# Kernel optimization log

Measured on AMD Instinct MI355X. Metric: run time of the kernel, lower is better.

Reference implementation:

```python
import jax, jax.numpy as jnp
import numpy as np

N_NODES = 8192
N_EDGES = 262144
FEAT = 128


def _lin(key, fan_in, fan_out):
    k1, k2 = jax.random.split(key)
    s = 1.0 / np.sqrt(fan_in)
    w = jax.random.uniform(k1, (fan_in, fan_out), jnp.float32, -s, s)
    b = jax.random.uniform(k2, (fan_out,), jnp.float32, -s, s)
    return w, b


def setup_inputs() -> dict:
    key = jax.random.key(0)
    ks = jax.random.split(key, 16)
    adj = jax.random.randint(ks[0], (2, N_EDGES), 0, N_NODES)
    features = jax.random.normal(ks[1], (N_NODES, FEAT), jnp.float32)
    w1, b1 = _lin(ks[2], FEAT, 64)
    w2, b2 = _lin(ks[3], 64, 32)
    w3, b3 = _lin(ks[4], 32, 32)
    # MultiheadAttention params (embed_dim=32, 1 head)
    kq = jax.random.split(ks[5], 2)
    wqkv = jax.random.uniform(kq[0], (96, 32), jnp.float32, -1/np.sqrt(32), 1/np.sqrt(32))
    bqkv = jnp.zeros((96,), jnp.float32)
    wo = jax.random.uniform(kq[1], (32, 32), jnp.float32, -1/np.sqrt(32), 1/np.sqrt(32))
    bo = jnp.zeros((32,), jnp.float32)
    w4, b4 = _lin(ks[6], 32, 32)
    w5a, b5a = _lin(ks[7], 32, 32)
    w6a, b6a = _lin(ks[8], 32, 64)
    w7a, b7a = _lin(ks[9], 64, 2)
    w5f, b5f = _lin(ks[10], 32, 32)
    w6f, b6f = _lin(ks[11], 32, 64)
    w7f, b7f = _lin(ks[12], 64, FEAT)
    return dict(adj=adj, features=features, w1=w1, b1=b1, w2=w2, b2=b2, w3=w3, b3=b3,
                wqkv=wqkv, bqkv=bqkv, wo=wo, bo=bo, w4=w4, b4=b4,
                w5a=w5a, b5a=b5a, w6a=w6a, b6a=b6a, w7a=w7a, b7a=b7a,
                w5f=w5f, b5f=b5f, w6f=w6f, b6f=b6f, w7f=w7f, b7f=b7f)


def _gcn(x, w, b, src, dst, norm, n):
    # PyG GCNConv: out = scatter_add(norm * (x W)[src] -> dst) + b
    h = x @ w
    return jax.ops.segment_sum(h[src] * norm[:, None], dst, num_segments=n) + b


def reference(adj, features, w1, b1, w2, b2, w3, b3, wqkv, bqkv, wo, bo, w4, b4,
              w5a, b5a, w6a, b6a, w7a, b7a, w5f, b5f, w6f, b6f, w7f, b7f):
    n = features.shape[0]
    loops = jnp.arange(n)
    src = jnp.concatenate([adj[0], loops])  # self-loops added (gcn_norm)
    dst = jnp.concatenate([adj[1], loops])
    deg = jax.ops.segment_sum(jnp.ones_like(src, jnp.float32), dst, num_segments=n)
    dinv = jnp.where(deg > 0, jax.lax.rsqrt(deg), 0.0)
    norm = dinv[src] * dinv[dst]

    h = jax.nn.relu(_gcn(features, w1, b1, src, dst, norm, n))
    h = jax.nn.relu(_gcn(h, w2, b2, src, dst, norm, n))
    h = jax.nn.relu(_gcn(h, w3, b3, src, dst, norm, n))

    # single-head self-attention over all nodes (seq_len=n, batch=1)
    qkv = h @ wqkv.T + bqkv
    q, k, v = jnp.split(qkv, 3, axis=-1)  # [n,32] each
    attn = jax.nn.softmax((q @ k.T) * (1.0 / np.sqrt(32.0)), axis=-1)  # [n,n]
    h = (attn @ v) @ wo.T + bo

    h = jax.nn.relu(_gcn(h, w4, b4, src, dst, norm, n))

    da = jax.nn.relu(_gcn(h, w5a, b5a, src, dst, norm, n))
    da = jax.nn.relu(_gcn(da, w6a, b6a, src, dst, norm, n))
    da = jax.nn.relu(_gcn(da, w7a, b7a, src, dst, norm, n))  # [n,2]

    df = jax.nn.relu(_gcn(h, w5f, b5f, src, dst, norm, n))
    df = jax.nn.relu(_gcn(df, w6f, b6f, src, dst, norm, n))
    df = jax.nn.relu(_gcn(df, w7f, b7f, src, dst, norm, n))  # [n,FEAT]
    return (da, df)
```

## Files before the change

### kernel.cpp

```cpp
#include <hip/hip_runtime.h>

#define N_NODES 8192
#define N_EDGES 262144

typedef __attribute__((ext_vector_type(4))) float f32x4;
typedef _Float16 half8 __attribute__((ext_vector_type(8)));
typedef _Float16 half4v __attribute__((ext_vector_type(4)));
typedef __fp16 fp16x2 __attribute__((ext_vector_type(2)));
union UH { half8 h8; fp16x2 h2[4]; };
union HC { _Float16 h; unsigned short u; };


__global__ void __launch_bounds__(256) zero_kernel(int4* __restrict__ p) {
  p[blockIdx.x * 256 + threadIdx.x] = make_int4(0, 0, 0, 0);
}


__global__ void __launch_bounds__(256) count_kernel(const int* __restrict__ dst,
                                                    int* __restrict__ cnt) {
  int e = blockIdx.x * 256 + threadIdx.x;
  atomicAdd(&cnt[dst[e]], 1);
}

__global__ void __launch_bounds__(1024) scan_kernel(const int* __restrict__ cnt,
                                                    int* __restrict__ rp,
                                                    float* __restrict__ dinv) {
  __shared__ int sums[1024];
  const int t = threadIdx.x;
  const int base = t * 8;
  int c[8];
  int s = 0;
#pragma unroll
  for (int i = 0; i < 8; ++i) { c[i] = cnt[base + i]; s += c[i]; }
  sums[t] = s;
  __syncthreads();
  for (int off = 1; off < 1024; off <<= 1) {
    int v = (t >= off) ? sums[t - off] : 0;
    __syncthreads();
    sums[t] += v;
    __syncthreads();
  }
  int run = (t == 0) ? 0 : sums[t - 1];
#pragma unroll
  for (int i = 0; i < 8; ++i) {
    rp[base + i] = run;
    run += c[i];
    dinv[base + i] = rsqrtf((float)(c[i] + 1));
  }
  if (t == 1023) rp[N_NODES] = run;
}

__global__ void __launch_bounds__(256) fill_kernel(const int* __restrict__ src,
                                                   const int* __restrict__ dst,
                                                   const int* __restrict__ rp,
                                                   const float* __restrict__ dinv,
                                                   int* __restrict__ cur,
                                                   int* __restrict__ col,
                                                   float* __restrict__ wgt) {
  int e = blockIdx.x * 256 + threadIdx.x;
  int d = dst[e], s = src[e];
  int p = atomicAdd(&cur[d], 1);
  int at = rp[d] + p;
  col[at] = s;
  wgt[at] = dinv[s] * dinv[d];
}


template <int FIN, int FOUT, bool WT, bool BIAS, bool RELU, bool O16>
__device__ __forceinline__ void mm_body(const float* __restrict__ x,
                                        const float* __restrict__ w,
                                        const float* __restrict__ bias, void* out,
                                        int bx, int tid, float* ws, float* xs) {
  constexpr int VEC = (FOUT >= 32) ? 4 : 1;
  constexpr int TC = FOUT / VEC;
  constexpr int ROWS = 256 / TC;
  const int r0 = bx * ROWS;
  for (int i = tid; i < FIN * FOUT; i += 256) {
    int k = i / FOUT, j = i % FOUT;
    ws[i] = WT ? w[j * FIN + k] : w[i];
  }
  for (int i = tid; i < ROWS * FIN; i += 256) {
    int r = i / FIN, k = i % FIN;
    xs[r * (FIN + 1) + k] = x[(size_t)(r0 + r) * FIN + k];
  }
  __syncthreads();
  const int jc = tid % TC, r = tid / TC;
  float acc[VEC];
#pragma unroll
  for (int v = 0; v < VEC; ++v) acc[v] = 0.0f;
#pragma unroll
  for (int k = 0; k < FIN; ++k) {
    const float xv = xs[r * (FIN + 1) + k];
#pragma unroll
    for (int v = 0; v < VEC; ++v) acc[v] += xv * ws[k * FOUT + jc * VEC + v];
  }
  float oval[VEC];
#pragma unroll
  for (int v = 0; v < VEC; ++v) {
    int j = jc * VEC + v;
    float o = BIAS ? (acc[v] + bias[j]) : acc[v];
    if (RELU) o = fmaxf(o, 0.0f);
    oval[v] = o;
  }
  if constexpr (O16 && VEC == 4) {
    unsigned short* o16 = (unsigned short*)out;
    half4v pk;
#pragma unroll
    for (int v = 0; v < 4; ++v) pk[v] = (_Float16)oval[v];
    *(half4v*)&o16[(size_t)(r0 + r) * FOUT + jc * 4] = pk;
  } else {
    float* of = (float*)out;
#pragma unroll
    for (int v = 0; v < VEC; ++v) of[(size_t)(r0 + r) * FOUT + jc * VEC + v] = oval[v];
  }
}

template <int FIN, int FOUT, bool WT, bool BIAS, bool RELU = false, bool O16 = false>
__global__ void __launch_bounds__(256) mm_kernel(const float* __restrict__ x,
                                                 const float* __restrict__ w,
                                                 const float* __restrict__ bias,
                                                 void* out) {
  constexpr int VEC = (FOUT >= 32) ? 4 : 1;
  constexpr int ROWS = 256 / (FOUT / VEC);
  __shared__ float ws[FIN * FOUT];
  __shared__ float xs[ROWS * (FIN + 1)];
  mm_body<FIN, FOUT, WT, BIAS, RELU, O16>(x, w, bias, out, blockIdx.x, threadIdx.x, ws, xs);
}

template <int FIN, int FOUT, bool WT, bool BIAS, bool RELU, int G, bool O16A = false,
          bool O16B = false>
__global__ void __launch_bounds__(256) mm_dual_kernel(
    const float* __restrict__ xA, const float* __restrict__ wA,
    const float* __restrict__ bA, void* outA,
    const float* __restrict__ xB, const float* __restrict__ wB,
    const float* __restrict__ bB, void* outB) {
  constexpr int VEC = (FOUT >= 32) ? 4 : 1;
  constexpr int ROWS = 256 / (FOUT / VEC);
  __shared__ float ws[FIN * FOUT];
  __shared__ float xs[ROWS * (FIN + 1)];
  if (blockIdx.x < G)
    mm_body<FIN, FOUT, WT, BIAS, RELU, O16A>(xA, wA, bA, outA, blockIdx.x, threadIdx.x, ws, xs);
  else
    mm_body<FIN, FOUT, WT, BIAS, RELU, O16B>(xB, wB, bB, outB, blockIdx.x - G, threadIdx.x, ws,
                                             xs);
}


template <int F, bool BR, bool I16, bool O16>
__device__ __forceinline__ void aggv_body(const void* __restrict__ t,
                                          const int* __restrict__ rp,
                                          const int* __restrict__ col,
                                          const float* __restrict__ wgt,
                                          const float* __restrict__ dinv,
                                          const float* __restrict__ bias,
                                          void* __restrict__ out, int bx, int tid) {
  constexpr int FPL = I16 ? 8 : 4;
  constexpr int TPN = F / FPL;
  constexpr int EPI = 64 / TPN;
  const int wv = tid >> 6;
  const int lane = tid & 63;
  const int n = bx * 4 + wv;
  const int eo = lane / TPN;
  const int fq = lane % TPN;
  const float di = dinv[n];
  const int rs = rp[n], re = rp[n + 1];
  float acc[FPL];
#pragma unroll
  for (int i = 0; i < FPL; ++i) acc[i] = 0.f;

  auto accum = [&](int node, float w) {
    if constexpr (I16) {
      const half8 hv = *(const half8*)((const unsigned short*)t + (size_t)node * F + fq * 8);
#pragma unroll
      for (int i = 0; i < 8; ++i) acc[i] += w * (float)hv[i];
    } else {
      const f32x4 v = *(const f32x4*)((const float*)t + (size_t)node * F + fq * 4);
#pragma unroll
      for (int i = 0; i < 4; ++i) acc[i] += w * v[i];
    }
  };
  if (eo == 0) accum(n, di * di);
  for (int e = rs + eo; e < re; e += EPI) {
    accum(col[e], wgt[e]);
  }
#pragma unroll
  for (int off = TPN; off < 64; off <<= 1) {
#pragma unroll
    for (int i = 0; i < FPL; ++i) acc[i] += __shfl_xor(acc[i], off, 64);
  }
  if (eo == 0) {
    float r[FPL];
#pragma unroll
    for (int i = 0; i < FPL; ++i) {
      float v = acc[i];
      if (BR) v = fmaxf(v + bias[fq * FPL + i], 0.f);
      r[i] = v;
    }
    if constexpr (O16) {
      unsigned short* o = (unsigned short*)out;
      if constexpr (FPL == 8) {
        half8 pk;
#pragma unroll
        for (int i = 0; i < 8; ++i) pk[i] = (_Float16)r[i];
        *(half8*)&o[(size_t)n * F + fq * 8] = pk;
      } else {
        half4v pk;
#pragma unroll
        for (int i = 0; i < 4; ++i) pk[i] = (_Float16)r[i];
        *(half4v*)&o[(size_t)n * F + fq * 4] = pk;
      }
    } else {
      float* o = (float*)out;
#pragma unroll
      for (int i = 0; i < FPL; i += 4)
        *(f32x4*)&o[(size_t)n * F + fq * FPL + i] = f32x4{r[i], r[i + 1], r[i + 2], r[i + 3]};
    }
  }
}

template <int F, bool BR = true, bool I16 = false, bool O16 = false>
__global__ void __launch_bounds__(256) aggv_kernel(const void* __restrict__ t,
                                                   const int* __restrict__ rp,
                                                   const int* __restrict__ col,
                                                   const float* __restrict__ wgt,
                                                   const float* __restrict__ dinv,
                                                   const float* __restrict__ bias,
                                                   void* __restrict__ out) {
  aggv_body<F, BR, I16, O16>(t, rp, col, wgt, dinv, bias, out, blockIdx.x, threadIdx.x);
}

template <int F, bool BR, bool I16, bool O16, int G>
__global__ void __launch_bounds__(256) aggv_dual_kernel(
    const void* __restrict__ tA, const float* __restrict__ bA, void* __restrict__ outA,
    const void* __restrict__ tB, const float* __restrict__ bB, void* __restrict__ outB,
    const int* __restrict__ rp, const int* __restrict__ col,
    const float* __restrict__ wgt, const float* __restrict__ dinv) {
  if (blockIdx.x < G)
    aggv_body<F, BR, I16, O16>(tA, rp, col, wgt, dinv, bA, outA, blockIdx.x, threadIdx.x);
  else
    aggv_body<F, BR, I16, O16>(tB, rp, col, wgt, dinv, bB, outB, blockIdx.x - G, threadIdx.x);
}

template <int F>
__global__ void __launch_bounds__(256) agg_kernel(const float* __restrict__ t,
                                                  const int* __restrict__ rp,
                                                  const int* __restrict__ col,
                                                  const float* __restrict__ wgt,
                                                  const float* __restrict__ dinv,
                                                  const float* __restrict__ bias,
                                                  float* __restrict__ out) {
  constexpr int NPB = 256 / F;
  const int tid = threadIdx.x;
  const int n = blockIdx.x * NPB + tid / F;
  const int f = tid % F;
  const float di = dinv[n];
  float acc = di * di * t[(size_t)n * F + f];
  const int rs = rp[n], re = rp[n + 1];
  for (int e = rs; e < re; ++e) {
    acc += wgt[e] * t[(size_t)col[e] * F + f];
  }
  acc += bias[f];
  out[(size_t)n * F + f] = fmaxf(acc, 0.0f);
}


__global__ void __launch_bounds__(256) qkv_kernel(const float* __restrict__ x,
                                                  const float* __restrict__ wqkv,
                                                  const float* __restrict__ bqkv,
                                                  unsigned short* __restrict__ Q16,
                                                  unsigned short* __restrict__ K16,
                                                  unsigned short* __restrict__ V16) {
  __shared__ float wls[96 * 33];
  __shared__ float xs[8 * 33];
  const int tid = threadIdx.x;
  const int r = tid >> 5, j = tid & 31;
  const int row = blockIdx.x * 8 + r;
  for (int i = tid; i < 96 * 32; i += 256) wls[(i >> 5) * 33 + (i & 31)] = wqkv[i];
  xs[(tid >> 5) * 33 + (tid & 31)] = x[(size_t)(blockIdx.x * 8 + (tid >> 5)) * 32 + (tid & 31)];
  __syncthreads();
  float aq = bqkv[j], ak = bqkv[32 + j], av = bqkv[64 + j];
#pragma unroll
  for (int k = 0; k < 32; ++k) {
    const float xv = xs[r * 33 + k];
    aq += xv * wls[j * 33 + k];
    ak += xv * wls[(32 + j) * 33 + k];
    av += xv * wls[(64 + j) * 33 + k];
  }
  const float QSCALE = 1.4426950408889634f * 0.17677669529663687f;
  aq *= QSCALE;
  HC cq, ck, cv;
  cq.h = (_Float16)aq;
  ck.h = (_Float16)ak;
  cv.h = (_Float16)av;
  Q16[row * 32 + j] = cq.u;
  K16[row * 32 + j] = ck.u;
  const int ko = row & 31;
  const int slot = 8 * ((ko & 15) >> 2) + ((ko >> 4) << 2) + (ko & 3);
  V16[j * N_NODES + (row & ~31) + slot] = cv.u;
}


__device__ __forceinline__ void wave_writeout(float (*lds)[544], float (*wexp)[16],
                                              float* Mq, float* Lq, const f32x4& o1,
                                              const f32x4& o2, float m, float l, int wid,
                                              int g, int li, int tid, int qt, int by,
                                              float* __restrict__ part) {
#pragma unroll
  for (int r = 0; r < 4; ++r) {
    lds[wid][(4 * g + r) * 16 + li] = o1[r];
    lds[wid][(16 + 4 * g + r) * 16 + li] = o2[r];
  }
  if (g == 0) {
    lds[wid][512 + li] = m;
    lds[wid][528 + li] = l;
  }
  __syncthreads();
  if (tid < 16) {
    const int q = tid;
    const float m0 = lds[0][512 + q], m1 = lds[1][512 + q];
    const float m2 = lds[2][512 + q], m3 = lds[3][512 + q];
    const float M = fmaxf(fmaxf(m0, m1), fmaxf(m2, m3));
    const float w0 = exp2f(m0 - M), w1 = exp2f(m1 - M);
    const float w2 = exp2f(m2 - M), w3 = exp2f(m3 - M);
    wexp[0][q] = w0; wexp[1][q] = w1; wexp[2][q] = w2; wexp[3][q] = w3;
    Mq[q] = M;
    Lq[q] = w0 * lds[0][528 + q] + w1 * lds[1][528 + q] +
            w2 * lds[2][528 + q] + w3 * lds[3][528 + q];
  }
  __syncthreads();
  const int base = (qt * 4 + by) * 544;
#pragma unroll
  for (int e2 = 0; e2 < 2; ++e2) {
    const int e = tid + e2 * 256;
    const int q = e & 15;
    part[base + e] = wexp[0][q] * lds[0][e] + wexp[1][q] * lds[1][e] +
                     wexp[2][q] * lds[2][e] + wexp[3][q] * lds[3][e];
  }
  if (tid < 16) {
    part[base + 512 + tid] = Mq[tid];
    part[base + 528 + tid] = Lq[tid];
  }
}

__global__ void __launch_bounds__(256, 4) attn_mfma_kernel(
    const unsigned short* __restrict__ Q16, const unsigned short* __restrict__ K16,
    const unsigned short* __restrict__ V16, float* __restrict__ part) {
  __shared__ float lds[4][544];
  __shared__ float wexp[4][16];
  __shared__ float Mq[16], Lq[16];
  const int tid = threadIdx.x;
  const int wid = tid >> 6;
  const int lane = tid & 63;
  const int g = lane >> 4;
  const int li = lane & 15;
  const int qpair = blockIdx.x;
  const int q0A = qpair * 32;
  const int q0B = q0A + 16;
  const int kbeg = blockIdx.y * 2048 + wid * 512;

  const half8 qfA = *(const half8*)&Q16[(q0A + li) * 32 + 8 * g];
  const half8 qfB = *(const half8*)&Q16[(q0B + li) * 32 + 8 * g];
  const int koff = li * 32 + 8 * g;
  const int vA = li * N_NODES + 8 * g;
  const int vB = (16 + li) * N_NODES + 8 * g;

  f32x4 oAA = {0.f, 0.f, 0.f, 0.f}, oBA = {0.f, 0.f, 0.f, 0.f};
  f32x4 oAB = {0.f, 0.f, 0.f, 0.f}, oBB = {0.f, 0.f, 0.f, 0.f};
  float mA = -1e30f, lA = 0.f, mB = -1e30f, lB = 0.f;

  for (int t = kbeg; t < kbeg + 512; t += 64) {
    const half8 k0 = *(const half8*)&K16[(t)*32 + koff];
    const half8 k1 = *(const half8*)&K16[(t + 16) * 32 + koff];
    const half8 k2 = *(const half8*)&K16[(t + 32) * 32 + koff];
    const half8 k3 = *(const half8*)&K16[(t + 48) * 32 + koff];
    const half8 va0 = *(const half8*)&V16[vA + t];
    const half8 vb0 = *(const half8*)&V16[vB + t];
    const half8 va1 = *(const half8*)&V16[vA + t + 32];
    const half8 vb1 = *(const half8*)&V16[vB + t + 32];

    {
      f32x4 s0 = {0.f, 0.f, 0.f, 0.f}, s1 = {0.f, 0.f, 0.f, 0.f};
      f32x4 s2 = {0.f, 0.f, 0.f, 0.f}, s3 = {0.f, 0.f, 0.f, 0.f};
      s0 = __builtin_amdgcn_mfma_f32_16x16x32_f16(k0, qfA, s0, 0, 0, 0);
      s1 = __builtin_amdgcn_mfma_f32_16x16x32_f16(k1, qfA, s1, 0, 0, 0);
      s2 = __builtin_amdgcn_mfma_f32_16x16x32_f16(k2, qfA, s2, 0, 0, 0);
      s3 = __builtin_amdgcn_mfma_f32_16x16x32_f16(k3, qfA, s3, 0, 0, 0);
      float mxl = fmaxf(fmaxf(fmaxf(s0[0], s0[1]), fmaxf(s0[2], s0[3])),
                        fmaxf(fmaxf(s1[0], s1[1]), fmaxf(s1[2], s1[3])));
      mxl = fmaxf(mxl, fmaxf(fmaxf(fmaxf(s2[0], s2[1]), fmaxf(s2[2], s2[3])),
                             fmaxf(fmaxf(s3[0], s3[1]), fmaxf(s3[2], s3[3]))));
      if (!__all(mxl <= mA)) {
        float mx = mxl;
        mx = fmaxf(mx, __shfl_xor(mx, 16, 64));
        mx = fmaxf(mx, __shfl_xor(mx, 32, 64));
        const float mn = fmaxf(mA, mx);
        const float fct = exp2f(mA - mn);
        oAA *= fct; oBA *= fct; lA *= fct;
        mA = mn;
      }
      const float p0 = exp2f(s0[0] - mA), p1 = exp2f(s0[1] - mA);
      const float p2 = exp2f(s0[2] - mA), p3 = exp2f(s0[3] - mA);
      const float p4 = exp2f(s1[0] - mA), p5 = exp2f(s1[1] - mA);
      const float p6 = exp2f(s1[2] - mA), p7 = exp2f(s1[3] - mA);
      const float p8 = exp2f(s2[0] - mA), p9 = exp2f(s2[1] - mA);
      const float pa = exp2f(s2[2] - mA), pb = exp2f(s2[3] - mA);
      const float pc = exp2f(s3[0] - mA), pd = exp2f(s3[1] - mA);
      const float pe = exp2f(s3[2] - mA), pf = exp2f(s3[3] - mA);
      lA += (((p0 + p1) + (p2 + p3)) + ((p4 + p5) + (p6 + p7))) +
            (((p8 + p9) + (pa + pb)) + ((pc + pd) + (pe + pf)));
      UH ph0, ph1;
      ph0.h2[0] = __builtin_amdgcn_cvt_pkrtz(p0, p1);
      ph0.h2[1] = __builtin_amdgcn_cvt_pkrtz(p2, p3);
      ph0.h2[2] = __builtin_amdgcn_cvt_pkrtz(p4, p5);
      ph0.h2[3] = __builtin_amdgcn_cvt_pkrtz(p6, p7);
      ph1.h2[0] = __builtin_amdgcn_cvt_pkrtz(p8, p9);
      ph1.h2[1] = __builtin_amdgcn_cvt_pkrtz(pa, pb);
      ph1.h2[2] = __builtin_amdgcn_cvt_pkrtz(pc, pd);
      ph1.h2[3] = __builtin_amdgcn_cvt_pkrtz(pe, pf);
      oAA = __builtin_amdgcn_mfma_f32_16x16x32_f16(va0, ph0.h8, oAA, 0, 0, 0);
      oAA = __builtin_amdgcn_mfma_f32_16x16x32_f16(va1, ph1.h8, oAA, 0, 0, 0);
      oBA = __builtin_amdgcn_mfma_f32_16x16x32_f16(vb0, ph0.h8, oBA, 0, 0, 0);
      oBA = __builtin_amdgcn_mfma_f32_16x16x32_f16(vb1, ph1.h8, oBA, 0, 0, 0);
    }
    {
      f32x4 s0 = {0.f, 0.f, 0.f, 0.f}, s1 = {0.f, 0.f, 0.f, 0.f};
      f32x4 s2 = {0.f, 0.f, 0.f, 0.f}, s3 = {0.f, 0.f, 0.f, 0.f};
      s0 = __builtin_amdgcn_mfma_f32_16x16x32_f16(k0, qfB, s0, 0, 0, 0);
      s1 = __builtin_amdgcn_mfma_f32_16x16x32_f16(k1, qfB, s1, 0, 0, 0);
      s2 = __builtin_amdgcn_mfma_f32_16x16x32_f16(k2, qfB, s2, 0, 0, 0);
      s3 = __builtin_amdgcn_mfma_f32_16x16x32_f16(k3, qfB, s3, 0, 0, 0);
      float mxl = fmaxf(fmaxf(fmaxf(s0[0], s0[1]), fmaxf(s0[2], s0[3])),
                        fmaxf(fmaxf(s1[0], s1[1]), fmaxf(s1[2], s1[3])));
      mxl = fmaxf(mxl, fmaxf(fmaxf(fmaxf(s2[0], s2[1]), fmaxf(s2[2], s2[3])),
                             fmaxf(fmaxf(s3[0], s3[1]), fmaxf(s3[2], s3[3]))));
      if (!__all(mxl <= mB)) {
        float mx = mxl;
        mx = fmaxf(mx, __shfl_xor(mx, 16, 64));
        mx = fmaxf(mx, __shfl_xor(mx, 32, 64));
        const float mn = fmaxf(mB, mx);
        const float fct = exp2f(mB - mn);
        oAB *= fct; oBB *= fct; lB *= fct;
        mB = mn;
      }
      const float p0 = exp2f(s0[0] - mB), p1 = exp2f(s0[1] - mB);
      const float p2 = exp2f(s0[2] - mB), p3 = exp2f(s0[3] - mB);
      const float p4 = exp2f(s1[0] - mB), p5 = exp2f(s1[1] - mB);
      const float p6 = exp2f(s1[2] - mB), p7 = exp2f(s1[3] - mB);
      const float p8 = exp2f(s2[0] - mB), p9 = exp2f(s2[1] - mB);
      const float pa = exp2f(s2[2] - mB), pb = exp2f(s2[3] - mB);
      const float pc = exp2f(s3[0] - mB), pd = exp2f(s3[1] - mB);
      const float pe = exp2f(s3[2] - mB), pf = exp2f(s3[3] - mB);
      lB += (((p0 + p1) + (p2 + p3)) + ((p4 + p5) + (p6 + p7))) +
            (((p8 + p9) + (pa + pb)) + ((pc + pd) + (pe + pf)));
      UH ph0, ph1;
      ph0.h2[0] = __builtin_amdgcn_cvt_pkrtz(p0, p1);
      ph0.h2[1] = __builtin_amdgcn_cvt_pkrtz(p2, p3);
      ph0.h2[2] = __builtin_amdgcn_cvt_pkrtz(p4, p5);
      ph0.h2[3] = __builtin_amdgcn_cvt_pkrtz(p6, p7);
      ph1.h2[0] = __builtin_amdgcn_cvt_pkrtz(p8, p9);
      ph1.h2[1] = __builtin_amdgcn_cvt_pkrtz(pa, pb);
      ph1.h2[2] = __builtin_amdgcn_cvt_pkrtz(pc, pd);
      ph1.h2[3] = __builtin_amdgcn_cvt_pkrtz(pe, pf);
      oAB = __builtin_amdgcn_mfma_f32_16x16x32_f16(va0, ph0.h8, oAB, 0, 0, 0);
      oAB = __builtin_amdgcn_mfma_f32_16x16x32_f16(va1, ph1.h8, oAB, 0, 0, 0);
      oBB = __builtin_amdgcn_mfma_f32_16x16x32_f16(vb0, ph0.h8, oBB, 0, 0, 0);
      oBB = __builtin_amdgcn_mfma_f32_16x16x32_f16(vb1, ph1.h8, oBB, 0, 0, 0);
    }
  }

  lA += __shfl_xor(lA, 16, 64);
  lA += __shfl_xor(lA, 32, 64);
  lB += __shfl_xor(lB, 16, 64);
  lB += __shfl_xor(lB, 32, 64);

  wave_writeout(lds, wexp, Mq, Lq, oAA, oBA, mA, lA, wid, g, li, tid, qpair * 2,
                blockIdx.y, part);
  __syncthreads();
  wave_writeout(lds, wexp, Mq, Lq, oAB, oBB, mB, lB, wid, g, li, tid, qpair * 2 + 1,
                blockIdx.y, part);
}


__global__ void __launch_bounds__(256) attn_combine_wo(const float* __restrict__ part,
                                                       const float* __restrict__ wo,
                                                       const float* __restrict__ bo,
                                                       float* __restrict__ out) {
  __shared__ float wols[1024];
  __shared__ float bos[32];
  __shared__ float aos[4][16][33];
  const int tid = threadIdx.x;
  for (int i = tid; i < 1024; i += 256) wols[i] = wo[i];
  if (tid < 32) bos[tid] = bo[tid];
  const int wv = tid >> 6, lane = tid & 63;
  const int qt = blockIdx.x * 4 + wv;
  const int q = lane & 15, g = lane >> 4;
  const int pb = qt * 4 * 544;
  const float m0 = part[pb + 512 + q], m1 = part[pb + 544 + 512 + q];
  const float m2 = part[pb + 1088 + 512 + q], m3 = part[pb + 1632 + 512 + q];
  const float M = fmaxf(fmaxf(m0, m1), fmaxf(m2, m3));
  const float w0 = exp2f(m0 - M), w1 = exp2f(m1 - M);
  const float w2 = exp2f(m2 - M), w3 = exp2f(m3 - M);
  const float L = w0 * part[pb + 528 + q] + w1 * part[pb + 544 + 528 + q] +
                  w2 * part[pb + 1088 + 528 + q] + w3 * part[pb + 1632 + 528 + q];
  const float invL = 1.0f / L;
#pragma unroll
  for (int r = 0; r < 8; ++r) {
    const int d = g + 4 * r;
    const int o = d * 16 + q;
    const float ov = w0 * part[pb + o] + w1 * part[pb + 544 + o] +
                     w2 * part[pb + 1088 + o] + w3 * part[pb + 1632 + o];
    aos[wv][q][d] = ov * invL;
  }
  __syncthreads();
#pragma unroll
  for (int r = 0; r < 8; ++r) {
    const int dout = g + 4 * r;
    float acc = bos[dout];
#pragma unroll
    for (int k = 0; k < 32; ++k) acc += aos[wv][q][k] * wols[dout * 32 + k];
    out[(size_t)(qt * 16 + q) * 32 + dout] = acc;
  }
}


extern "C" void kernel_launch(void* const* d_in, const int* in_sizes, int n_in,
                              void* d_out, int out_size, void* d_ws, size_t ws_size,
                              hipStream_t stream) {
  (void)in_sizes; (void)n_in; (void)out_size; (void)ws_size;
  const int* adj = (const int*)d_in[0];
  const float* feat = (const float*)d_in[1];
  const float* w1 = (const float*)d_in[2];  const float* b1 = (const float*)d_in[3];
  const float* w2 = (const float*)d_in[4];  const float* b2 = (const float*)d_in[5];
  const float* w3 = (const float*)d_in[6];  const float* b3 = (const float*)d_in[7];
  const float* wqkv = (const float*)d_in[8];const float* bqkv = (const float*)d_in[9];
  const float* wo = (const float*)d_in[10]; const float* bo = (const float*)d_in[11];
  const float* w4 = (const float*)d_in[12]; const float* b4 = (const float*)d_in[13];
  const float* w5a = (const float*)d_in[14];const float* b5a = (const float*)d_in[15];
  const float* w6a = (const float*)d_in[16];const float* b6a = (const float*)d_in[17];
  const float* w7a = (const float*)d_in[18];const float* b7a = (const float*)d_in[19];
  const float* w5f = (const float*)d_in[20];const float* b5f = (const float*)d_in[21];
  const float* w6f = (const float*)d_in[22];const float* b6f = (const float*)d_in[23];
  const float* w7f = (const float*)d_in[24];const float* b7f = (const float*)d_in[25];
  float* outp = (float*)d_out;

  float* wsf = (float*)d_ws;
  int* wsi = (int*)d_ws;
  int* cnt = wsi;
  int* cur = wsi + 8192;
  int* rp = wsi + 16384;
  float* dinv = wsf + 24832;
  float* wgt = wsf + 33024;
  int* col = wsi + 295168;
  float* T = wsf + 557312;
  float* T2 = T + 262144;
  float* B0 = wsf + 1605888;
  float* B1 = wsf + 2130176;
  float* B2 = wsf + 2392320;
  unsigned short* Q16 = (unsigned short*)(wsf + 2916608);
  unsigned short* K16 = Q16 + 262144;
  unsigned short* V16 = K16 + 262144;
  unsigned short* T16 = (unsigned short*)T;
  unsigned short* B0h = (unsigned short*)B0;
  unsigned short* B1h = (unsigned short*)B1;
  unsigned short* B2h = (unsigned short*)B2;
  float* part = T;

  const int* src = adj;
  const int* dst = adj + N_EDGES;

  zero_kernel<<<16, 256, 0, stream>>>((int4*)cnt);
  count_kernel<<<N_EDGES / 256, 256, 0, stream>>>(dst, cnt);
  scan_kernel<<<1, 1024, 0, stream>>>(cnt, rp, dinv);
  fill_kernel<<<N_EDGES / 256, 256, 0, stream>>>(src, dst, rp, dinv, cur, col, wgt);

  mm_kernel<128, 64, false, false, false, true><<<N_NODES / 16, 256, 0, stream>>>(
      feat, w1, nullptr, T16);
  aggv_kernel<64, true, true, false><<<N_NODES / 4, 256, 0, stream>>>(T16, rp, col, wgt,
                                                                      dinv, b1, B0);
  mm_kernel<64, 32, false, false, false, true><<<N_NODES / 32, 256, 0, stream>>>(
      B0, w2, nullptr, T16);
  aggv_kernel<32, true, true, false><<<N_NODES / 4, 256, 0, stream>>>(T16, rp, col, wgt,
                                                                      dinv, b2, B1);
  mm_kernel<32, 32, false, false, false, true><<<N_NODES / 32, 256, 0, stream>>>(
      B1, w3, nullptr, T16);
  aggv_kernel<32, true, true, false><<<N_NODES / 4, 256, 0, stream>>>(T16, rp, col, wgt,
                                                                      dinv, b3, B0);

  qkv_kernel<<<N_NODES / 8, 256, 0, stream>>>(B0, wqkv, bqkv, Q16, K16, V16);
  {
    dim3 grid(256, 4);
    attn_mfma_kernel<<<grid, 256, 0, stream>>>(Q16, K16, V16, part);
  }
  attn_combine_wo<<<128, 256, 0, stream>>>(part, wo, bo, B2);

  mm_kernel<32, 32, false, false, false, true><<<N_NODES / 32, 256, 0, stream>>>(
      B2, w4, nullptr, T16);
  aggv_kernel<32, true, true, true><<<N_NODES / 4, 256, 0, stream>>>(T16, rp, col, wgt,
                                                                     dinv, b4, B0h);

  aggv_kernel<32, false, true, false><<<N_NODES / 4, 256, 0, stream>>>(B0h, rp, col, wgt,
                                                                       dinv, nullptr, T);
  mm_dual_kernel<32, 32, false, true, true, 256, true, true><<<512, 256, 0, stream>>>(
      T, w5a, b5a, B1h, T, w5f, b5f, B2h);
  aggv_dual_kernel<32, false, true, false, 2048><<<4096, 256, 0, stream>>>(
      B1h, nullptr, T, B2h, nullptr, T2, rp, col, wgt, dinv);
  mm_dual_kernel<32, 64, false, true, true, 512, false, true><<<1024, 256, 0, stream>>>(
      T, w6a, b6a, B0, T2, w6f, b6f, B2h);
  mm_kernel<64, 2, false, false><<<N_NODES / 128, 256, 0, stream>>>(B0, w7a, nullptr, B1);
  agg_kernel<2><<<N_NODES / 128, 256, 0, stream>>>(B1, rp, col, wgt, dinv, b7a, outp);
  aggv_kernel<64, false, true, false><<<N_NODES / 4, 256, 0, stream>>>(B2h, rp, col, wgt,
                                                                       dinv, nullptr, T);
  mm_kernel<64, 128, false, true, true><<<N_NODES / 8, 256, 0, stream>>>(T, w7f, b7f,
                                                                         outp + 16384);
}
```

Before: 191.7 us.

## Fuse launches: edge count with first matmul, wo with w4, tail branches

The degree-count atomics now run in the same launch as the first feature matmul, as extra blocks of one kernel. The zeroing of the fill cursor moves into the scan kernel, and the zero kernel covers only the count array. The attention combine kernel now also applies the w4 projection and writes fp16 directly, removing a separate matmul launch and a round trip through global memory. The two final output branches are merged into two heterogeneous kernels that run independent matmul and aggregation work side by side. Together these cut launch count and tail serialization, at the cost of more shared memory per block and mixed block roles within one grid.

```diff
diff --git a/kernel.cpp b/kernel.cpp
--- a/kernel.cpp
+++ b/kernel.cpp
@@ -16,22 +16,17 @@
 }
 
 
-__global__ void __launch_bounds__(256) count_kernel(const int* __restrict__ dst,
-                                                    int* __restrict__ cnt) {
-  int e = blockIdx.x * 256 + threadIdx.x;
-  atomicAdd(&cnt[dst[e]], 1);
-}
-
 __global__ void __launch_bounds__(1024) scan_kernel(const int* __restrict__ cnt,
                                                     int* __restrict__ rp,
-                                                    float* __restrict__ dinv) {
+                                                    float* __restrict__ dinv,
+                                                    int* __restrict__ cur) {
   __shared__ int sums[1024];
   const int t = threadIdx.x;
   const int base = t * 8;
   int c[8];
   int s = 0;
 #pragma unroll
-  for (int i = 0; i < 8; ++i) { c[i] = cnt[base + i]; s += c[i]; }
+  for (int i = 0; i < 8; ++i) { c[i] = cnt[base + i]; s += c[i]; cur[base + i] = 0; }
   sums[t] = s;
   __syncthreads();
   for (int off = 1; off < 1024; off <<= 1) {
@@ -241,26 +236,62 @@
     aggv_body<F, BR, I16, O16>(tB, rp, col, wgt, dinv, bB, outB, blockIdx.x - G, threadIdx.x);
 }
 
-template <int F>
-__global__ void __launch_bounds__(256) agg_kernel(const float* __restrict__ t,
-                                                  const int* __restrict__ rp,
-                                                  const int* __restrict__ col,
-                                                  const float* __restrict__ wgt,
-                                                  const float* __restrict__ dinv,
-                                                  const float* __restrict__ bias,
-                                                  float* __restrict__ out) {
-  constexpr int NPB = 256 / F;
-  const int tid = threadIdx.x;
-  const int n = blockIdx.x * NPB + tid / F;
-  const int f = tid % F;
-  const float di = dinv[n];
-  float acc = di * di * t[(size_t)n * F + f];
-  const int rs = rp[n], re = rp[n + 1];
-  for (int e = rs; e < re; ++e) {
-    acc += wgt[e] * t[(size_t)col[e] * F + f];
-  }
-  acc += bias[f];
-  out[(size_t)n * F + f] = fmaxf(acc, 0.0f);
+
+__global__ void __launch_bounds__(256) cm_kernel(const int* __restrict__ dst,
+                                                 int* __restrict__ cnt,
+                                                 const float* __restrict__ feat,
+                                                 const float* __restrict__ w1,
+                                                 unsigned short* __restrict__ T16) {
+  __shared__ float ws[128 * 64];
+  __shared__ float xs[16 * 129];
+  if (blockIdx.x < 512) {
+    mm_body<128, 64, false, false, false, true>(feat, w1, nullptr, T16, blockIdx.x,
+                                                threadIdx.x, ws, xs);
+  } else {
+    int e = (blockIdx.x - 512) * 256 + threadIdx.x;
+    atomicAdd(&cnt[dst[e]], 1);
+  }
+}
+
+__global__ void __launch_bounds__(256) het1_kernel(
+    const float* __restrict__ h6a, const float* __restrict__ w7a, float* __restrict__ pre7a,
+    const unsigned short* __restrict__ h6f, float* __restrict__ g7f,
+    const int* __restrict__ rp, const int* __restrict__ col,
+    const float* __restrict__ wgt, const float* __restrict__ dinv) {
+  __shared__ float ws[64 * 2];
+  __shared__ float xs[128 * 65];
+  if (blockIdx.x < 64)
+    mm_body<64, 2, false, false, false, false>(h6a, w7a, nullptr, pre7a, blockIdx.x,
+                                               threadIdx.x, ws, xs);
+  else
+    aggv_body<64, false, true, false>(h6f, rp, col, wgt, dinv, nullptr, g7f,
+                                      blockIdx.x - 64, threadIdx.x);
+}
+
+__global__ void __launch_bounds__(256) het2_kernel(
+    const float* __restrict__ pre7a, const float* __restrict__ b7a, float* __restrict__ outa,
+    const float* __restrict__ g7f, const float* __restrict__ w7f,
+    const float* __restrict__ b7f, float* __restrict__ outf,
+    const int* __restrict__ rp, const int* __restrict__ col,
+    const float* __restrict__ wgt, const float* __restrict__ dinv) {
+  __shared__ float ws[64 * 128];
+  __shared__ float xs[8 * 65];
+  if (blockIdx.x < 64) {
+    const int tid = threadIdx.x;
+    const int n = blockIdx.x * 128 + tid / 2;
+    const int f = tid & 1;
+    const float di = dinv[n];
+    float acc = di * di * pre7a[(size_t)n * 2 + f];
+    const int rs = rp[n], re = rp[n + 1];
+    for (int e = rs; e < re; ++e) {
+      acc += wgt[e] * pre7a[(size_t)col[e] * 2 + f];
+    }
+    acc += b7a[f];
+    outa[(size_t)n * 2 + f] = fmaxf(acc, 0.0f);
+  } else {
+    mm_body<64, 128, false, true, true, false>(g7f, w7f, b7f, outf, blockIdx.x - 64,
+                                               threadIdx.x, ws, xs);
+  }
 }
 
 
@@ -481,15 +512,21 @@
 }
 
 
-__global__ void __launch_bounds__(256) attn_combine_wo(const float* __restrict__ part,
-                                                       const float* __restrict__ wo,
-                                                       const float* __restrict__ bo,
-                                                       float* __restrict__ out) {
+__global__ void __launch_bounds__(256) attn_combine_wo_w4(const float* __restrict__ part,
+                                                          const float* __restrict__ wo,
+                                                          const float* __restrict__ bo,
+                                                          const float* __restrict__ w4,
+                                                          unsigned short* __restrict__ T16out) {
   __shared__ float wols[1024];
+  __shared__ float w4ls[1024];
   __shared__ float bos[32];
   __shared__ float aos[4][16][33];
+  __shared__ float hs[4][16][33];
   const int tid = threadIdx.x;
-  for (int i = tid; i < 1024; i += 256) wols[i] = wo[i];
+  for (int i = tid; i < 1024; i += 256) {
+    wols[i] = wo[i];
+    w4ls[i] = w4[i];
+  }
   if (tid < 32) bos[tid] = bo[tid];
   const int wv = tid >> 6, lane = tid & 63;
   const int qt = blockIdx.x * 4 + wv;
@@ -518,7 +555,17 @@
     float acc = bos[dout];
 #pragma unroll
     for (int k = 0; k < 32; ++k) acc += aos[wv][q][k] * wols[dout * 32 + k];
-    out[(size_t)(qt * 16 + q) * 32 + dout] = acc;
+    hs[wv][q][dout] = acc;
+  }
+#pragma unroll
+  for (int r = 0; r < 8; ++r) {
+    const int dout = g + 4 * r;
+    float acc = 0.f;
+#pragma unroll
+    for (int k = 0; k < 32; ++k) acc += hs[wv][q][k] * w4ls[k * 32 + dout];
+    HC c;
+    c.h = (_Float16)acc;
+    T16out[(size_t)(qt * 16 + q) * 32 + dout] = c.u;
   }
 }
 
@@ -568,13 +615,11 @@
   const int* src = adj;
   const int* dst = adj + N_EDGES;
 
-  zero_kernel<<<16, 256, 0, stream>>>((int4*)cnt);
-  count_kernel<<<N_EDGES / 256, 256, 0, stream>>>(dst, cnt);
-  scan_kernel<<<1, 1024, 0, stream>>>(cnt, rp, dinv);
+  zero_kernel<<<8, 256, 0, stream>>>((int4*)cnt);
+  cm_kernel<<<1536, 256, 0, stream>>>(dst, cnt, feat, w1, T16);
+  scan_kernel<<<1, 1024, 0, stream>>>(cnt, rp, dinv, cur);
   fill_kernel<<<N_EDGES / 256, 256, 0, stream>>>(src, dst, rp, dinv, cur, col, wgt);
 
-  mm_kernel<128, 64, false, false, false, true><<<N_NODES / 16, 256, 0, stream>>>(
-      feat, w1, nullptr, T16);
   aggv_kernel<64, true, true, false><<<N_NODES / 4, 256, 0, stream>>>(T16, rp, col, wgt,
                                                                       dinv, b1, B0);
   mm_kernel<64, 32, false, false, false, true><<<N_NODES / 32, 256, 0, stream>>>(
@@ -591,10 +636,8 @@
     dim3 grid(256, 4);
     attn_mfma_kernel<<<grid, 256, 0, stream>>>(Q16, K16, V16, part);
   }
-  attn_combine_wo<<<128, 256, 0, stream>>>(part, wo, bo, B2);
-
-  mm_kernel<32, 32, false, false, false, true><<<N_NODES / 32, 256, 0, stream>>>(
-      B2, w4, nullptr, T16);
+  attn_combine_wo_w4<<<128, 256, 0, stream>>>(part, wo, bo, w4, T16);
+
   aggv_kernel<32, true, true, true><<<N_NODES / 4, 256, 0, stream>>>(T16, rp, col, wgt,
                                                                      dinv, b4, B0h);
 
@@ -606,10 +649,7 @@
       B1h, nullptr, T, B2h, nullptr, T2, rp, col, wgt, dinv);
   mm_dual_kernel<32, 64, false, true, true, 512, false, true><<<1024, 256, 0, stream>>>(
       T, w6a, b6a, B0, T2, w6f, b6f, B2h);
-  mm_kernel<64, 2, false, false><<<N_NODES / 128, 256, 0, stream>>>(B0, w7a, nullptr, B1);
-  agg_kernel<2><<<N_NODES / 128, 256, 0, stream>>>(B1, rp, col, wgt, dinv, b7a, outp);
-  aggv_kernel<64, false, true, false><<<N_NODES / 4, 256, 0, stream>>>(B2h, rp, col, wgt,
-                                                                       dinv, nullptr, T);
-  mm_kernel<64, 128, false, true, true><<<N_NODES / 8, 256, 0, stream>>>(T, w7f, b7f,
-                                                                         outp + 16384);
-}
+  het1_kernel<<<64 + 2048, 256, 0, stream>>>(B0, w7a, B1, B2h, T, rp, col, wgt, dinv);
+  het2_kernel<<<64 + 1024, 256, 0, stream>>>(B1, b7a, outp, T, w7f, b7f, outp + 16384, rp,
+                                             col, wgt, dinv);
+}
```

New measurement: 179.4 us. 6.4% less time.
